# Performance work log

Measured on AMD Instinct MI355X. Metric: run time of the kernel, lower is better.

The kernel has to match this reference:

```python
import jax, jax.numpy as jnp
import numpy as np

N_NODES = 100000
N_EDGES = 3200000
D = 32


def _gat(x, edge_index, W, att_s, att_d, bias, heads, ch, neg_slope):
    """PyG-style GATConv (shared lin for src/dst, add_self_loops=False).
    x: [N, D_in], edge_index: [2, E], W: [heads*ch, D_in],
    att_s/att_d: [heads, ch], bias: [heads*ch]. Returns [N, heads*ch]."""
    n = x.shape[0]
    h = (x @ W.T).reshape(n, heads, ch)                      # [N,H,C]
    a_s = (h * att_s[None]).sum(-1)                           # [N,H]
    a_d = (h * att_d[None]).sum(-1)                           # [N,H]
    src, dst = edge_index[0], edge_index[1]
    logits = jax.nn.leaky_relu(a_s[src] + a_d[dst], neg_slope)  # [E,H]
    # segment softmax over edges grouped by destination node
    m = jax.ops.segment_max(logits, dst, num_segments=n)     # [N,H]
    m = jnp.where(jnp.isfinite(m), m, 0.0)                    # nodes w/ no in-edges
    ex = jnp.exp(logits - m[dst])                             # [E,H]
    denom = jax.ops.segment_sum(ex, dst, num_segments=n)     # [N,H]
    alpha = ex / (denom[dst] + 1e-16)                         # [E,H]
    out = jax.ops.segment_sum(alpha[:, :, None] * h[src], dst, num_segments=n)  # [N,H,C]
    return out.reshape(n, heads * ch) + bias


def setup_inputs() -> dict:
    key = jax.random.key(0)
    ks = jax.random.split(key, 16)
    x = jax.random.normal(ks[0], (N_NODES, D), dtype=jnp.float32)
    edge_index = jax.random.randint(ks[1], (2, N_EDGES), 0, N_NODES, dtype=jnp.int64)
    s = 1.0 / np.sqrt(D)
    return {
        "x": x,
        "edge_index": edge_index,
        "W1": jax.random.normal(ks[2], (32, D), dtype=jnp.float32) * s,
        "att_s1": jax.random.normal(ks[3], (2, 16), dtype=jnp.float32) * 0.05,
        "att_d1": jax.random.normal(ks[4], (2, 16), dtype=jnp.float32) * 0.05,
        "b1": jnp.full((32,), 0.1, dtype=jnp.float32),
        "ea1": jnp.ones((1,), dtype=jnp.float32),  # edge_activator
        "W2": jax.random.normal(ks[5], (32, 32), dtype=jnp.float32) * s,
        "att_s2": jax.random.normal(ks[6], (2, 16), dtype=jnp.float32) * 0.05,
        "att_d2": jax.random.normal(ks[7], (2, 16), dtype=jnp.float32) * 0.05,
        "b2": jnp.full((32,), 0.1, dtype=jnp.float32),
        "W3": jax.random.normal(ks[8], (32, 32), dtype=jnp.float32) * s,
        "att_s3": jax.random.normal(ks[9], (1, 32), dtype=jnp.float32) * 0.05,
        "att_d3": jax.random.normal(ks[10], (1, 32), dtype=jnp.float32) * 0.05,
        "b3": jnp.full((32,), 0.1, dtype=jnp.float32),
    }


def reference(x, edge_index, W1, att_s1, att_d1, b1, ea1,
              W2, att_s2, att_d2, b2, W3, att_s3, att_d3, b3):
    # --- layer 1 (negative_slope=0.01) ---
    h = _gat(x, edge_index, W1, att_s1, att_d1, b1, heads=2, ch=16, neg_slope=0.01)
    scale = jnp.tanh(ea1)[0]
    scale = jnp.where(scale < 0.1, 1.0, scale)  # 'continue' branch skips the scaling
    h = h * scale
    h = h + 0.05 * jax.lax.stop_gradient(h)      # h + 0.05*h.detach()
    h = jax.nn.elu(h)                            # eval path (training=False)
    h = jnp.clip(h, -3.0, 3.0)
    # --- layer 2 (default negative_slope=0.2) ---
    h = _gat(h, edge_index, W2, att_s2, att_d2, b2, heads=2, ch=16, neg_slope=0.2)
    h = jax.nn.elu(h)
    h = jnp.clip(h, -3.0, 3.0)
    # --- layer 3: heads=1, concat=False ---
    out = _gat(h, edge_index, W3, att_s3, att_d3, b3, heads=1, ch=32, neg_slope=0.2)
    return out
```

## Files before the change

### kernel.cpp

```cpp
#include <hip/hip_runtime.h>
#include <hip/hip_bf16.h>
#include <hip/hip_fp16.h>


#define NPB  128
#define CAPB 6144
#define PAD_SENTINEL 0xFFFFFFFFu

__global__ void k_initcur(int* __restrict__ cursor, int nb) {
    int i = blockIdx.x * 256 + threadIdx.x;
    if (i < nb) cursor[i] = i * CAPB;
}

__global__ void __launch_bounds__(1024)
k_bin(const int* __restrict__ src, const int* __restrict__ dst,
      int* __restrict__ bucket_cursor, unsigned int* __restrict__ pairs,
      int e, int nb) {
    const int EPT = 8;
    __shared__ int h[1024];
    __shared__ int cbase[1024];
    __shared__ int room[1024];
    int t = threadIdx.x;
    for (int i = t; i < nb; i += 1024) h[i] = 0;
    __syncthreads();
    int e4 = e >> 2;
    int base4 = blockIdx.x * 2048;
    int boff[EPT];
    unsigned int pk[EPT];
#pragma unroll
    for (int k = 0; k < 2; k++) {
        int i4 = base4 + k * 1024 + t;
        if (i4 < e4) {
            int4 dv = ((const int4*)dst)[i4];
            int4 sv = ((const int4*)src)[i4];
            const int* dd = (const int*)&dv;
            const int* ss = (const int*)&sv;
#pragma unroll
            for (int j = 0; j < 4; j++) {
                int q = 4 * k + j;
                int d = dd[j];
                int b = d >> 7;
                pk[q] = ((unsigned int)ss[j] << 7) | (unsigned int)(d & 127);
                int off = atomicAdd(&h[b], 1);
                boff[q] = (b << 16) | off;
            }
        } else {
#pragma unroll
            for (int j = 0; j < 4; j++) boff[4 * k + j] = -1;
        }
    }
    __syncthreads();
    for (int i = t; i < nb; i += 1024) {
        int c = h[i];
        if (c) {
            int r = (c + 7) & ~7;
            int cb = atomicAdd(&bucket_cursor[i], r);
            int rm = (i + 1) * CAPB - cb;
            cbase[i] = cb;
            room[i] = rm;
            for (int j = c; j < r && j < rm; j++)
                pairs[cb + j] = PAD_SENTINEL;
        }
    }
    __syncthreads();
#pragma unroll
    for (int q = 0; q < EPT; q++) {
        if (boff[q] >= 0) {
            int b = boff[q] >> 16;
            int off = boff[q] & 0xFFFF;
            if (off < room[b]) pairs[cbase[b] + off] = pk[q];
        }
    }
    if (blockIdx.x == 0 && t < (e & 3)) {
        int i = (e & ~3) + t;
        int d = dst[i];
        int b = d >> 7;
        int pos = atomicAdd(&bucket_cursor[b], 1);
        if (pos < (b + 1) * CAPB)
            pairs[pos] = ((unsigned int)src[i] << 7) | (unsigned int)(d & 127);
    }
}

__global__ void __launch_bounds__(512)
k_bucket_sort(const unsigned int* __restrict__ pairs,
              const int* __restrict__ bucket_cursor,
              int2* __restrict__ rowinfo, int* __restrict__ src_sorted,
              int n) {
    __shared__ int cnt[NPB];
    __shared__ int cur[NPB];
    __shared__ int total;
    __shared__ unsigned int lp[CAPB];
    __shared__ int op[CAPB];
    int b = blockIdx.x;
    int t = threadIdx.x;
    int bbase = b * CAPB;
    int m = bucket_cursor[b] - bbase;
    if (m > CAPB) m = CAPB;
    if (t < NPB) cnt[t] = 0;
    __syncthreads();
    for (int cb = 0; cb < m; cb += 4096) {
        unsigned int pv[8];
#pragma unroll
        for (int u = 0; u < 8; u++) {
            int i = cb + u * 512 + t;
            pv[u] = (i < m) ? pairs[bbase + i] : PAD_SENTINEL;
        }
#pragma unroll
        for (int u = 0; u < 8; u++) {
            int i = cb + u * 512 + t;
            if (i < m) lp[i] = pv[u];
            if (pv[u] != PAD_SENTINEL) atomicAdd(&cnt[pv[u] & 127], 1);
        }
    }
    __syncthreads();
    if (t < 64) {
        int c0 = cnt[2 * t];
        int c1 = cnt[2 * t + 1];
        int sum = c0 + c1;
        int run = sum;
#pragma unroll
        for (int off = 1; off < 64; off <<= 1) {
            int v = __shfl_up(run, off, 64);
            if (t >= off) run += v;
        }
        int ex = run - sum;
        cur[2 * t] = ex;
        cur[2 * t + 1] = ex + c0;
        int node = b * NPB + 2 * t;
        if (node < n) rowinfo[node] = make_int2(bbase + ex, c0);
        if (node + 1 < n) rowinfo[node + 1] = make_int2(bbase + ex + c0, c1);
        if (t == 63) total = run;
    }
    __syncthreads();
    for (int cb = 0; cb < m; cb += 4096) {
        unsigned int pv[8];
        int of[8];
#pragma unroll
        for (int u = 0; u < 8; u++) {
            int i = cb + u * 512 + t;
            pv[u] = (i < m) ? lp[i] : PAD_SENTINEL;
        }
#pragma unroll
        for (int u = 0; u < 8; u++)
            if (pv[u] != PAD_SENTINEL) of[u] = atomicAdd(&cur[pv[u] & 127], 1);
#pragma unroll
        for (int u = 0; u < 8; u++)
            if (pv[u] != PAD_SENTINEL) op[of[u]] = (int)(pv[u] >> 7);
    }
    __syncthreads();
    int nt4 = (total + 3) >> 2;
    int4* dst4 = (int4*)(src_sorted + bbase);
    const int4* src4 = (const int4*)op;
    for (int i = t; i < nt4; i += 512) dst4[i] = src4[i];
}

template <int H>
__global__ void k_transform(const float* __restrict__ in, const float* __restrict__ W,
                            const float* __restrict__ att_s, const float* __restrict__ att_d,
                            __half* __restrict__ h16, float* __restrict__ a_s,
                            float* __restrict__ a_d, int n) {
    constexpr int C = 32 / H;
    __shared__ float Wl[32][33];
    __shared__ float xs[8][32];
    int t = threadIdx.x;
    for (int i = t; i < 1024; i += 256) Wl[i >> 5][i & 31] = W[i];
    int nl = t >> 5, o = t & 31;
    int node = blockIdx.x * 8 + nl;
    xs[nl][o] = (node < n) ? in[node * 32 + o] : 0.f;
    __syncthreads();
    float acc = 0.f;
#pragma unroll
    for (int k = 0; k < 32; k++) acc = fmaf(xs[nl][k], Wl[o][k], acc);
    if (node < n) {
        h16[node * 32 + o] = __float2half_rn(acc);
        float vs = acc * att_s[o];
        float vd = acc * att_d[o];
#pragma unroll
        for (int m = C / 2; m >= 1; m >>= 1) {
            vs += __shfl_xor(vs, m, 64);
            vd += __shfl_xor(vd, m, 64);
        }
        if ((o % C) == 0) {
            int hh = o / C;
            a_s[node * H + hh] = vs;
            a_d[node * H + hh] = vd;
        }
    }
}

template <int H, int EPI>
__global__ void k_edge(const int2* __restrict__ rowinfo, const int* __restrict__ src_sorted,
                       const __half* __restrict__ h16,
                       const float* __restrict__ a_s, const float* __restrict__ a_d,
                       const float* __restrict__ bias, const float* __restrict__ ea,
                       float* __restrict__ out, int n, float slope) {
    constexpr int CAP = 128;
    constexpr int RSTR = 2 * CAP + 16;
    __shared__ int lds_raw[8][H][RSTR];
    int nw = threadIdx.x >> 5;
    int hl = threadIdx.x & 31;
    int node = blockIdx.x * 8 + nw;
    if (node >= n) return;
    int2 bi = rowinfo[node];
    int beg = bi.x, deg = bi.y;
    int padB = (deg + 15) & ~15;

    float ad[H];
#pragma unroll
    for (int hh = 0; hh < H; hh++) ad[hh] = a_d[node * H + hh];

    float ds[H];
#pragma unroll
    for (int hh = 0; hh < H; hh++) ds[hh] = 0.f;
    bool fast = (padB <= CAP);
    if (fast) {
        for (int idx = hl; idx < padB; idx += 32) {
            if (idx < deg) {
                int s = src_sorted[beg + idx];
                if (H == 2) {
                    float2 as2 = *(const float2*)((const char*)a_s + (unsigned)(s << 3));
                    float l0 = as2.x + ad[0]; l0 = fmaxf(l0, l0 * slope);
                    float l1 = as2.y + ad[1]; l1 = fmaxf(l1, l1 * slope);
                    float e0 = __expf(l0), e1 = __expf(l1);
                    ds[0] += e0; ds[1] += e1;
                    ((int2*)lds_raw[nw][0])[idx] = make_int2(s, __float_as_int(e0));
                    ((int2*)lds_raw[nw][H - 1])[idx] = make_int2(s, __float_as_int(e1));
                } else {
                    float l0 = a_s[s] + ad[0]; l0 = fmaxf(l0, l0 * slope);
                    float e0 = __expf(l0);
                    ds[0] += e0;
                    ((int2*)lds_raw[nw][0])[idx] = make_int2(s, __float_as_int(e0));
                }
            } else {
#pragma unroll
                for (int hh = 0; hh < H; hh++)
                    ((int2*)lds_raw[nw][hh])[idx] = make_int2(0, 0);
            }
        }
    } else {
        for (int idx = hl; idx < deg; idx += 32) {
            int s = src_sorted[beg + idx];
            if (H == 2) {
                float2 as2 = *(const float2*)((const char*)a_s + (unsigned)(s << 3));
                float l0 = as2.x + ad[0]; l0 = fmaxf(l0, l0 * slope);
                float l1 = as2.y + ad[1]; l1 = fmaxf(l1, l1 * slope);
                ds[0] += __expf(l0); ds[1] += __expf(l1);
            } else {
                float l0 = a_s[s] + ad[0]; l0 = fmaxf(l0, l0 * slope);
                ds[0] += __expf(l0);
            }
        }
    }

    int e2 = hl >> 4;
    int l16 = hl & 15;
    int hd = (H == 2) ? (l16 >> 3) : 0;
    int co = l16 << 2;
    float adh = ad[hd];
    float acc0 = 0.f, acc1 = 0.f;
    const char* hbase = (const char*)h16;
    const int* lb = &lds_raw[nw][hd][e2 * 4];

    if (fast) {
        for (int base = 0; base < padB; base += 16) {
            int4 qa = *(const int4*)(lb + base * 2);
            int4 qb = *(const int4*)(lb + base * 2 + 8);
            int4 qc = *(const int4*)(lb + base * 2 + 16);
            int4 qd = *(const int4*)(lb + base * 2 + 24);
            __half2 h0 = *(const __half2*)(hbase + (unsigned)((qa.x << 6) + co));
            __half2 h1 = *(const __half2*)(hbase + (unsigned)((qa.z << 6) + co));
            __half2 h2 = *(const __half2*)(hbase + (unsigned)((qb.x << 6) + co));
            __half2 h3 = *(const __half2*)(hbase + (unsigned)((qb.z << 6) + co));
            __half2 h4 = *(const __half2*)(hbase + (unsigned)((qc.x << 6) + co));
            __half2 h5 = *(const __half2*)(hbase + (unsigned)((qc.z << 6) + co));
            __half2 h6 = *(const __half2*)(hbase + (unsigned)((qd.x << 6) + co));
            __half2 h7 = *(const __half2*)(hbase + (unsigned)((qd.z << 6) + co));
            float xa0 = __int_as_float(qa.y), xa1 = __int_as_float(qa.w);
            float xb0 = __int_as_float(qb.y), xb1 = __int_as_float(qb.w);
            float xc0 = __int_as_float(qc.y), xc1 = __int_as_float(qc.w);
            float xd0 = __int_as_float(qd.y), xd1 = __int_as_float(qd.w);
            acc0 = fmaf(xa0, __half2float(__low2half(h0)), acc0);
            acc1 = fmaf(xa0, __half2float(__high2half(h0)), acc1);
            acc0 = fmaf(xa1, __half2float(__low2half(h1)), acc0);
            acc1 = fmaf(xa1, __half2float(__high2half(h1)), acc1);
            acc0 = fmaf(xb0, __half2float(__low2half(h2)), acc0);
            acc1 = fmaf(xb0, __half2float(__high2half(h2)), acc1);
            acc0 = fmaf(xb1, __half2float(__low2half(h3)), acc0);
            acc1 = fmaf(xb1, __half2float(__high2half(h3)), acc1);
            acc0 = fmaf(xc0, __half2float(__low2half(h4)), acc0);
            acc1 = fmaf(xc0, __half2float(__high2half(h4)), acc1);
            acc0 = fmaf(xc1, __half2float(__low2half(h5)), acc0);
            acc1 = fmaf(xc1, __half2float(__high2half(h5)), acc1);
            acc0 = fmaf(xd0, __half2float(__low2half(h6)), acc0);
            acc1 = fmaf(xd0, __half2float(__high2half(h6)), acc1);
            acc0 = fmaf(xd1, __half2float(__low2half(h7)), acc0);
            acc1 = fmaf(xd1, __half2float(__high2half(h7)), acc1);
        }
    } else {
        for (int base = 0; base < deg; base += 16) {
#pragma unroll
            for (int u = 0; u < 8; u++) {
                int idx = base + u * 2 + e2;
                int s = 0;
                float ex = 0.f;
                if (idx < deg) {
                    s = src_sorted[beg + idx];
                    float l = a_s[s * H + hd] + adh;
                    l = fmaxf(l, l * slope);
                    ex = __expf(l);
                }
                __half2 hv = *(const __half2*)(hbase + (unsigned)((s << 6) + co));
                acc0 = fmaf(ex, __half2float(__low2half(hv)), acc0);
                acc1 = fmaf(ex, __half2float(__high2half(hv)), acc1);
            }
        }
    }

#pragma unroll
    for (int hh = 0; hh < H; hh++) {
        float v = ds[hh];
#pragma unroll
        for (int m = 16; m >= 1; m >>= 1) v += __shfl_xor(v, m, 64);
        ds[hh] = 1.f / (v + 1e-16f);
    }

    acc0 += __shfl_xor(acc0, 16, 64);
    acc1 += __shfl_xor(acc1, 16, 64);

    if (l16 == hl) {
        float invd = ds[hd];
        float2 bv = *(const float2*)(bias + l16 * 2);
        float v0 = fmaf(acc0, invd, bv.x);
        float v1 = fmaf(acc1, invd, bv.y);
        if (EPI == 1) {
            float s0 = tanhf(ea[0]);
            if (s0 < 0.1f) s0 = 1.0f;
            s0 *= 1.05f;
            v0 *= s0; v1 *= s0;
            v0 = (v0 > 0.f) ? v0 : expm1f(v0);
            v1 = (v1 > 0.f) ? v1 : expm1f(v1);
            v0 = fminf(3.f, fmaxf(-3.f, v0));
            v1 = fminf(3.f, fmaxf(-3.f, v1));
        } else if (EPI == 2) {
            v0 = (v0 > 0.f) ? v0 : expm1f(v0);
            v1 = (v1 > 0.f) ? v1 : expm1f(v1);
            v0 = fminf(3.f, fmaxf(-3.f, v0));
            v1 = fminf(3.f, fmaxf(-3.f, v1));
        }
        *(float2*)(out + (size_t)node * 32 + l16 * 2) = make_float2(v0, v1);
    }
}

extern "C" void kernel_launch(void* const* d_in, const int* in_sizes, int n_in,
                              void* d_out, int out_size, void* d_ws, size_t ws_size,
                              hipStream_t stream) {
    const float* x   = (const float*)d_in[0];
    const int*   ei  = (const int*)d_in[1];
    const float* W1  = (const float*)d_in[2];
    const float* as1 = (const float*)d_in[3];
    const float* ad1 = (const float*)d_in[4];
    const float* b1  = (const float*)d_in[5];
    const float* ea1 = (const float*)d_in[6];
    const float* W2  = (const float*)d_in[7];
    const float* as2 = (const float*)d_in[8];
    const float* ad2 = (const float*)d_in[9];
    const float* b2  = (const float*)d_in[10];
    const float* W3  = (const float*)d_in[11];
    const float* as3 = (const float*)d_in[12];
    const float* ad3 = (const float*)d_in[13];
    const float* b3  = (const float*)d_in[14];
    float* out = (float*)d_out;

    const int n = in_sizes[0] / 32;
    const int e = in_sizes[1] / 2;
    const int* src = ei;
    const int* dst = ei + e;
    const int nb = (n + NPB - 1) / NPB;

    char* w = (char*)d_ws;
    auto alloc = [&](size_t bytes) -> void* {
        void* p = (void*)w;
        w += (bytes + 255) & ~(size_t)255;
        return p;
    };
    __half* h16     = (__half*)alloc((size_t)n * 32 * 2);
    float* a_s      = (float*)alloc((size_t)n * 2 * 4);
    float* a_d      = (float*)alloc((size_t)n * 2 * 4);
    float* bufA     = (float*)alloc((size_t)n * 32 * 4);
    float* bufB     = (float*)alloc((size_t)n * 32 * 4);
    int2* rowinfo   = (int2*)alloc((size_t)n * 8);
    int* bucket_cur = (int*)alloc((size_t)(nb + 1) * 4);
    int* src_sorted = (int*)alloc((size_t)nb * CAPB * 4);
    unsigned int* pairs = (unsigned int*)bufA;

    k_initcur<<<(nb + 255) / 256, 256, 0, stream>>>(bucket_cur, nb);
    int e4 = e >> 2;
    k_bin<<<(e4 + 2047) / 2048, 1024, 0, stream>>>(src, dst, bucket_cur, pairs, e, nb);
    k_bucket_sort<<<nb, 512, 0, stream>>>(pairs, bucket_cur, rowinfo, src_sorted, n);

    const int tgrid = (n + 7) / 8;
    const int egrid = (n + 7) / 8;

    k_transform<2><<<tgrid, 256, 0, stream>>>(x, W1, as1, ad1, h16, a_s, a_d, n);
    k_edge<2, 1><<<egrid, 256, 0, stream>>>(rowinfo, src_sorted, h16, a_s, a_d, b1, ea1, bufA, n, 0.01f);

    k_transform<2><<<tgrid, 256, 0, stream>>>(bufA, W2, as2, ad2, h16, a_s, a_d, n);
    k_edge<2, 2><<<egrid, 256, 0, stream>>>(rowinfo, src_sorted, h16, a_s, a_d, b2, nullptr, bufB, n, 0.2f);

    k_transform<1><<<tgrid, 256, 0, stream>>>(bufB, W3, as3, ad3, h16, a_s, a_d, n);
    k_edge<1, 0><<<egrid, 256, 0, stream>>>(rowinfo, src_sorted, h16, a_s, a_d, b3, nullptr, out, n, 0.2f);
}
```

Measured before the change: 338.7 us.

## Replicate bucket-sort counters, unroll edge gather to 32, memset cursors

Bucket cursors now hold offsets relative to each bucket, so they can be zeroed with hipMemsetAsync instead of a dedicated init kernel. The bucket-sort kernel keeps four replicated per-node counters to spread LDS atomic contention, then recombines them in the scan. The edge kernel's fast path processes 32 edges per iteration with all gathers issued before the FMAs, raising memory-level parallelism at the cost of more registers and padding the degree to a multiple of 32. The padding change may read LDS entries beyond those previously written, which relies on the fill stage zeroing up to the new pad.

```diff
diff --git a/kernel.cpp b/kernel.cpp
--- a/kernel.cpp
+++ b/kernel.cpp
@@ -6,11 +6,6 @@
 #define NPB  128
 #define CAPB 6144
 #define PAD_SENTINEL 0xFFFFFFFFu
-
-__global__ void k_initcur(int* __restrict__ cursor, int nb) {
-    int i = blockIdx.x * 256 + threadIdx.x;
-    if (i < nb) cursor[i] = i * CAPB;
-}
 
 __global__ void __launch_bounds__(1024)
 k_bin(const int* __restrict__ src, const int* __restrict__ dst,
@@ -54,12 +49,13 @@
         int c = h[i];
         if (c) {
             int r = (c + 7) & ~7;
-            int cb = atomicAdd(&bucket_cursor[i], r);
-            int rm = (i + 1) * CAPB - cb;
-            cbase[i] = cb;
+            int cbr = atomicAdd(&bucket_cursor[i], r);
+            int rm = CAPB - cbr;
+            int ab = i * CAPB + cbr;
+            cbase[i] = ab;
             room[i] = rm;
             for (int j = c; j < r && j < rm; j++)
-                pairs[cb + j] = PAD_SENTINEL;
+                pairs[ab + j] = PAD_SENTINEL;
         }
     }
     __syncthreads();
@@ -75,9 +71,9 @@
         int i = (e & ~3) + t;
         int d = dst[i];
         int b = d >> 7;
-        int pos = atomicAdd(&bucket_cursor[b], 1);
-        if (pos < (b + 1) * CAPB)
-            pairs[pos] = ((unsigned int)src[i] << 7) | (unsigned int)(d & 127);
+        int posr = atomicAdd(&bucket_cursor[b], 1);
+        if (posr < CAPB)
+            pairs[b * CAPB + posr] = ((unsigned int)src[i] << 7) | (unsigned int)(d & 127);
     }
 }
 
@@ -86,17 +82,18 @@
               const int* __restrict__ bucket_cursor,
               int2* __restrict__ rowinfo, int* __restrict__ src_sorted,
               int n) {
-    __shared__ int cnt[NPB];
-    __shared__ int cur[NPB];
+    __shared__ int cnt4[NPB][4];
+    __shared__ int cur4[NPB][4];
     __shared__ int total;
     __shared__ unsigned int lp[CAPB];
     __shared__ int op[CAPB];
     int b = blockIdx.x;
     int t = threadIdx.x;
+    int rep = t & 3;
     int bbase = b * CAPB;
-    int m = bucket_cursor[b] - bbase;
+    int m = bucket_cursor[b];
     if (m > CAPB) m = CAPB;
-    if (t < NPB) cnt[t] = 0;
+    if (t < NPB) { cnt4[t][0] = 0; cnt4[t][1] = 0; cnt4[t][2] = 0; cnt4[t][3] = 0; }
     __syncthreads();
     for (int cb = 0; cb < m; cb += 4096) {
         unsigned int pv[8];
@@ -109,13 +106,16 @@
         for (int u = 0; u < 8; u++) {
             int i = cb + u * 512 + t;
             if (i < m) lp[i] = pv[u];
-            if (pv[u] != PAD_SENTINEL) atomicAdd(&cnt[pv[u] & 127], 1);
+            if (pv[u] != PAD_SENTINEL) atomicAdd(&cnt4[pv[u] & 127][rep], 1);
         }
     }
     __syncthreads();
     if (t < 64) {
-        int c0 = cnt[2 * t];
-        int c1 = cnt[2 * t + 1];
+        int q0[4], q1[4];
+#pragma unroll
+        for (int j = 0; j < 4; j++) { q0[j] = cnt4[2 * t][j]; q1[j] = cnt4[2 * t + 1][j]; }
+        int c0 = q0[0] + q0[1] + q0[2] + q0[3];
+        int c1 = q1[0] + q1[1] + q1[2] + q1[3];
         int sum = c0 + c1;
         int run = sum;
 #pragma unroll
@@ -124,8 +124,11 @@
             if (t >= off) run += v;
         }
         int ex = run - sum;
-        cur[2 * t] = ex;
-        cur[2 * t + 1] = ex + c0;
+        int o = ex;
+#pragma unroll
+        for (int j = 0; j < 4; j++) { cur4[2 * t][j] = o; o += q0[j]; }
+#pragma unroll
+        for (int j = 0; j < 4; j++) { cur4[2 * t + 1][j] = o; o += q1[j]; }
         int node = b * NPB + 2 * t;
         if (node < n) rowinfo[node] = make_int2(bbase + ex, c0);
         if (node + 1 < n) rowinfo[node + 1] = make_int2(bbase + ex + c0, c1);
@@ -142,7 +145,7 @@
         }
 #pragma unroll
         for (int u = 0; u < 8; u++)
-            if (pv[u] != PAD_SENTINEL) of[u] = atomicAdd(&cur[pv[u] & 127], 1);
+            if (pv[u] != PAD_SENTINEL) of[u] = atomicAdd(&cur4[pv[u] & 127][rep], 1);
 #pragma unroll
         for (int u = 0; u < 8; u++)
             if (pv[u] != PAD_SENTINEL) op[of[u]] = (int)(pv[u] >> 7);
@@ -203,7 +206,7 @@
     if (node >= n) return;
     int2 bi = rowinfo[node];
     int beg = bi.x, deg = bi.y;
-    int padB = (deg + 15) & ~15;
+    int padB = (deg + 31) & ~31;
 
     float ad[H];
 #pragma unroll
@@ -262,39 +265,24 @@
     const int* lb = &lds_raw[nw][hd][e2 * 4];
 
     if (fast) {
-        for (int base = 0; base < padB; base += 16) {
-            int4 qa = *(const int4*)(lb + base * 2);
-            int4 qb = *(const int4*)(lb + base * 2 + 8);
-            int4 qc = *(const int4*)(lb + base * 2 + 16);
-            int4 qd = *(const int4*)(lb + base * 2 + 24);
-            __half2 h0 = *(const __half2*)(hbase + (unsigned)((qa.x << 6) + co));
-            __half2 h1 = *(const __half2*)(hbase + (unsigned)((qa.z << 6) + co));
-            __half2 h2 = *(const __half2*)(hbase + (unsigned)((qb.x << 6) + co));
-            __half2 h3 = *(const __half2*)(hbase + (unsigned)((qb.z << 6) + co));
-            __half2 h4 = *(const __half2*)(hbase + (unsigned)((qc.x << 6) + co));
-            __half2 h5 = *(const __half2*)(hbase + (unsigned)((qc.z << 6) + co));
-            __half2 h6 = *(const __half2*)(hbase + (unsigned)((qd.x << 6) + co));
-            __half2 h7 = *(const __half2*)(hbase + (unsigned)((qd.z << 6) + co));
-            float xa0 = __int_as_float(qa.y), xa1 = __int_as_float(qa.w);
-            float xb0 = __int_as_float(qb.y), xb1 = __int_as_float(qb.w);
-            float xc0 = __int_as_float(qc.y), xc1 = __int_as_float(qc.w);
-            float xd0 = __int_as_float(qd.y), xd1 = __int_as_float(qd.w);
-            acc0 = fmaf(xa0, __half2float(__low2half(h0)), acc0);
-            acc1 = fmaf(xa0, __half2float(__high2half(h0)), acc1);
-            acc0 = fmaf(xa1, __half2float(__low2half(h1)), acc0);
-            acc1 = fmaf(xa1, __half2float(__high2half(h1)), acc1);
-            acc0 = fmaf(xb0, __half2float(__low2half(h2)), acc0);
-            acc1 = fmaf(xb0, __half2float(__high2half(h2)), acc1);
-            acc0 = fmaf(xb1, __half2float(__low2half(h3)), acc0);
-            acc1 = fmaf(xb1, __half2float(__high2half(h3)), acc1);
-            acc0 = fmaf(xc0, __half2float(__low2half(h4)), acc0);
-            acc1 = fmaf(xc0, __half2float(__high2half(h4)), acc1);
-            acc0 = fmaf(xc1, __half2float(__low2half(h5)), acc0);
-            acc1 = fmaf(xc1, __half2float(__high2half(h5)), acc1);
-            acc0 = fmaf(xd0, __half2float(__low2half(h6)), acc0);
-            acc1 = fmaf(xd0, __half2float(__high2half(h6)), acc1);
-            acc0 = fmaf(xd1, __half2float(__low2half(h7)), acc0);
-            acc1 = fmaf(xd1, __half2float(__high2half(h7)), acc1);
+        for (int base = 0; base < padB; base += 32) {
+            int4 q[8];
+#pragma unroll
+            for (int k = 0; k < 8; k++) q[k] = *(const int4*)(lb + base * 2 + 8 * k);
+            __half2 hv[16];
+#pragma unroll
+            for (int k = 0; k < 8; k++) {
+                hv[2 * k]     = *(const __half2*)(hbase + (unsigned)((q[k].x << 6) + co));
+                hv[2 * k + 1] = *(const __half2*)(hbase + (unsigned)((q[k].z << 6) + co));
+            }
+#pragma unroll
+            for (int k = 0; k < 8; k++) {
+                float x0 = __int_as_float(q[k].y), x1 = __int_as_float(q[k].w);
+                acc0 = fmaf(x0, __half2float(__low2half(hv[2 * k])), acc0);
+                acc1 = fmaf(x0, __half2float(__high2half(hv[2 * k])), acc1);
+                acc0 = fmaf(x1, __half2float(__low2half(hv[2 * k + 1])), acc0);
+                acc1 = fmaf(x1, __half2float(__high2half(hv[2 * k + 1])), acc1);
+            }
         }
     } else {
         for (int base = 0; base < deg; base += 16) {
@@ -393,7 +381,7 @@
     int* src_sorted = (int*)alloc((size_t)nb * CAPB * 4);
     unsigned int* pairs = (unsigned int*)bufA;
 
-    k_initcur<<<(nb + 255) / 256, 256, 0, stream>>>(bucket_cur, nb);
+    hipMemsetAsync(bucket_cur, 0, (size_t)nb * 4, stream);
     int e4 = e >> 2;
     k_bin<<<(e4 + 2047) / 2048, 1024, 0, stream>>>(src, dst, bucket_cur, pairs, e, nb);
     k_bucket_sort<<<nb, 512, 0, stream>>>(pairs, bucket_cur, rowinfo, src_sorted, n);
```

Measured after the change: 344.1 us. About the same (+1.6%).
